# Kernel optimization log

Hardware: AMD Instinct MI355X
Metric: run time of the kernel (lower is better)

The kernel has to match this reference:

```python
import jax, jax.numpy as jnp
import numpy as np

B, N, D_IN, D_HID = 8, 2048, 512, 512

def setup_inputs() -> dict:
    key = jax.random.key(0)
    k1, k2, k3 = jax.random.split(key, 3)
    inp = jax.random.normal(k1, (B, N, D_IN), dtype=jnp.float32)
    # nn.Linear(input_size, hidden_size): weight [hidden, in], bias [hidden]
    W = jax.random.normal(k2, (D_HID, D_IN), dtype=jnp.float32) * (1.0 / np.sqrt(D_IN))
    b = jax.random.normal(k3, (D_HID,), dtype=jnp.float32) * 0.01
    return {"input": inp, "W": W, "b": b}

def reference(input, W, b):
    # x = fc(input): [B, N, D_HID]
    x = jnp.einsum('bnd,hd->bnh', input, W) + b
    # scores = x @ x^T (NO scale factor, matching the original): [B, N, N]
    scores = jnp.einsum('bnh,bmh->bnm', x, x)
    attn = jax.nn.softmax(scores, axis=2)
    # output = attn @ raw input (V = input, not the projection): [B, N, D_IN]
    output = jnp.einsum('bnm,bmd->bnd', attn, input)
    return output
```

## Files before the change

kernel.cpp:

```cpp
#include <hip/hip_runtime.h>
#include <hip/hip_bf16.h>
#include <stdint.h>

typedef short vbf16x8 __attribute__((ext_vector_type(8)));
typedef float vf32x4 __attribute__((ext_vector_type(4)));
typedef unsigned short u16;

__device__ __forceinline__ float bf2f(u16 u) {
  union { unsigned int i; float f; } v; v.i = ((unsigned int)u) << 16; return v.f;
}
__device__ __forceinline__ u16 f2bf(float f) {
  union { float f; unsigned int i; } v; v.f = f;
  return (u16)((v.i + 0x7fffu + ((v.i >> 16) & 1u)) >> 16);
}
__device__ __forceinline__ void gld16(const void* g, void* l) {
  __builtin_amdgcn_global_load_lds((const __attribute__((address_space(1))) void*)g,
                                   (__attribute__((address_space(3))) void*)l, 16, 0, 0);
}
template<int N> __device__ __forceinline__ void wait_vmcnt() {
  asm volatile("s_waitcnt vmcnt(%0)" :: "n"(N) : "memory");
}
__device__ __forceinline__ vbf16x8 ldsv(const u16* p) { return *(const vbf16x8*)p; }

__global__ __launch_bounds__(256) void k_convw(const float* __restrict__ W, u16* __restrict__ Wb) {
  int i = blockIdx.x * 256 + threadIdx.x;
  float4 x = ((const float4*)W)[i];
  ushort4 h;
  h.x = f2bf(x.x); h.y = f2bf(x.y); h.z = f2bf(x.z); h.w = f2bf(x.w);
  ((ushort4*)Wb)[i] = h;
}

__global__ __launch_bounds__(256) void k_prep(const float* __restrict__ in,
                                              u16* __restrict__ Abf, u16* __restrict__ Vt) {
  __shared__ u16 Ts[64][72];
  const int tid = threadIdx.x;
  const int n0 = blockIdx.x * 64, d0 = blockIdx.y * 64, b = blockIdx.z;
  const float* src = in + ((long long)b * 2048 + n0) * 512 + d0;
#pragma unroll
  for (int j = 0; j < 4; ++j) {
    int chunk = tid + 256 * j;
    int r = chunk >> 4, c = (chunk & 15) * 4;
    float4 x = *(const float4*)(src + (long long)r * 512 + c);
    ushort4 h;
    h.x = f2bf(x.x); h.y = f2bf(x.y); h.z = f2bf(x.z); h.w = f2bf(x.w);
    *(ushort4*)(Abf + ((long long)b * 2048 + n0 + r) * 512 + d0 + c) = h;
    Ts[c + 0][r] = h.x; Ts[c + 1][r] = h.y; Ts[c + 2][r] = h.z; Ts[c + 3][r] = h.w;
  }
  __syncthreads();
#pragma unroll
  for (int j = 0; j < 2; ++j) {
    int chunk = tid + 256 * j;
    int dr = chunk >> 3, c8 = (chunk & 7) * 8;
    vbf16x8 w = *(const vbf16x8*)&Ts[dr][c8];
    *(vbf16x8*)(Vt + ((long long)b * 512 + d0 + dr) * 2048 + n0 + c8) = w;
  }
}

template<int NF, int PART>
__device__ __forceinline__ void stage_part(int tile, int NT, const u16* gA, const u16* gB,
                                           u16* As, u16* Bs, int rA, int colsw, int K, int wv) {
  if (tile >= NT) return;
  constexpr int kh = PART >> 1;
  constexpr int isB = PART & 1;
  const int buf = tile & 1;
  const int k0 = tile * 64 + kh * 32;
  if constexpr (!isB) {
    const u16* src = gA + (long long)rA * K + k0 + colsw;
    u16* dst = As + (buf * 2 + kh) * 8192 + wv * 512;
    gld16(src, dst);
    gld16(src + 128LL * K, dst + 4096);
  } else {
    constexpr int BN = 64 * NF;
    const u16* src = gB + (long long)rA * K + k0 + colsw;
    u16* dst = Bs + (buf * 2 + kh) * (BN * 32) + wv * 512;
    gld16(src, dst);
    if constexpr (NF == 4) gld16(src + 128LL * K, dst + 4096);
  }
}

template<int NF, bool OUTBF, bool BIAS, int MAP>
__global__ __launch_bounds__(512, 2) void k_gemm8(const u16* __restrict__ A,
                                                  const u16* __restrict__ Bt,
                                                  const float* __restrict__ bias,
                                                  void* __restrict__ Cout,
                                                  int M, int N, int K,
                                                  long long sA, long long sB, long long sC) {
  static_assert(NF == 2 || NF == 4, "NF");
  constexpr int BN = 64 * NF;
  constexpr int LB = NF / 2;
  constexpr int V_MAIN = 4 + LB;
  constexpr int V_LAST = 2 + LB;
  __shared__ __align__(16) u16 As[2 * 2 * 256 * 32];
  __shared__ __align__(16) u16 Bs[2 * 2 * BN * 32];

  const int tid = threadIdx.x, lane = tid & 63, wv = tid >> 6;
  const int wr = wv >> 2, wc = wv & 3;

  const int lin = blockIdx.x;
  const int xcd = lin & 7, idx = lin >> 3;
  int zb, browi, bcoli;
  if constexpr (MAP == 0) { zb = xcd; browi = idx >> 3; bcoli = idx & 7; }
  else if constexpr (MAP == 1) { zb = 0; browi = xcd * 8 + (idx >> 2); bcoli = idx & 3; }
  else { zb = xcd; browi = idx >> 2; bcoli = idx & 3; }
  const int brow = browi * 256, bcol = bcoli * BN;
  const long long z = zb;

  const u16* gA = A + z * sA + (long long)brow * K;
  const u16* gB = Bt + z * sB + (long long)bcol * K;
  const int NT = K >> 6;

  const int rA = wv * 16 + (lane >> 2);
  const int colsw = (((lane & 3) ^ ((lane >> 3) & 3)) << 3);

  const int slotp = ((lane >> 4) ^ (((lane & 15) >> 1) & 3));
  const int rdoff = (lane & 15) * 32 + slotp * 8;

  vf32x4 acc[8][NF] = {};

  stage_part<NF, 0>(0, NT, gA, gB, As, Bs, rA, colsw, K, wv);
  stage_part<NF, 1>(0, NT, gA, gB, As, Bs, rA, colsw, K, wv);
  stage_part<NF, 2>(0, NT, gA, gB, As, Bs, rA, colsw, K, wv);
  stage_part<NF, 3>(0, NT, gA, gB, As, Bs, rA, colsw, K, wv);
  stage_part<NF, 0>(1, NT, gA, gB, As, Bs, rA, colsw, K, wv);

  for (int t = 0; t < NT; ++t) {
    const int buf = t & 1;
    const u16* Ak0 = As + (buf * 2 + 0) * 8192 + wr * 4096 + rdoff;
    const u16* Ak1 = As + (buf * 2 + 1) * 8192 + wr * 4096 + rdoff;
    const u16* Bk0 = Bs + (buf * 2 + 0) * (BN * 32) + wc * (16 * NF) * 32 + rdoff;
    const u16* Bk1 = Bs + (buf * 2 + 1) * (BN * 32) + wc * (16 * NF) * 32 + rdoff;
    vbf16x8 afr[4], bfr[NF];

    if (t < NT - 1) wait_vmcnt<V_MAIN>(); else wait_vmcnt<V_LAST>();
    __builtin_amdgcn_sched_barrier(0);
    __builtin_amdgcn_s_barrier();
    __builtin_amdgcn_sched_barrier(0);
#pragma unroll
    for (int n = 0; n < NF; ++n) bfr[n] = ldsv(Bk0 + n * 512);
#pragma unroll
    for (int i = 0; i < 4; ++i) afr[i] = ldsv(Ak0 + i * 512);
    stage_part<NF, 1>(t + 1, NT, gA, gB, As, Bs, rA, colsw, K, wv);
    __builtin_amdgcn_s_setprio(1);
#pragma unroll
    for (int i = 0; i < 4; ++i)
#pragma unroll
      for (int n = 0; n < NF; ++n)
        acc[i][n] = __builtin_amdgcn_mfma_f32_16x16x32_bf16(afr[i], bfr[n], acc[i][n], 0, 0, 0);
    __builtin_amdgcn_s_setprio(0);

#pragma unroll
    for (int i = 0; i < 4; ++i) afr[i] = ldsv(Ak0 + (4 + i) * 512);
    stage_part<NF, 2>(t + 1, NT, gA, gB, As, Bs, rA, colsw, K, wv);
    __builtin_amdgcn_s_setprio(1);
#pragma unroll
    for (int i = 0; i < 4; ++i)
#pragma unroll
      for (int n = 0; n < NF; ++n)
        acc[4 + i][n] = __builtin_amdgcn_mfma_f32_16x16x32_bf16(afr[i], bfr[n], acc[4 + i][n], 0, 0, 0);
    __builtin_amdgcn_s_setprio(0);

    if (t < NT - 1) wait_vmcnt<V_MAIN>(); else wait_vmcnt<0>();
    __builtin_amdgcn_sched_barrier(0);
    __builtin_amdgcn_s_barrier();
    __builtin_amdgcn_sched_barrier(0);
#pragma unroll
    for (int n = 0; n < NF; ++n) bfr[n] = ldsv(Bk1 + n * 512);
#pragma unroll
    for (int i = 0; i < 4; ++i) afr[i] = ldsv(Ak1 + i * 512);
    stage_part<NF, 3>(t + 1, NT, gA, gB, As, Bs, rA, colsw, K, wv);
    __builtin_amdgcn_s_setprio(1);
#pragma unroll
    for (int i = 0; i < 4; ++i)
#pragma unroll
      for (int n = 0; n < NF; ++n)
        acc[i][n] = __builtin_amdgcn_mfma_f32_16x16x32_bf16(afr[i], bfr[n], acc[i][n], 0, 0, 0);
    __builtin_amdgcn_s_setprio(0);

#pragma unroll
    for (int i = 0; i < 4; ++i) afr[i] = ldsv(Ak1 + (4 + i) * 512);
    stage_part<NF, 0>(t + 2, NT, gA, gB, As, Bs, rA, colsw, K, wv);
    __builtin_amdgcn_s_setprio(1);
#pragma unroll
    for (int i = 0; i < 4; ++i)
#pragma unroll
      for (int n = 0; n < NF; ++n)
        acc[4 + i][n] = __builtin_amdgcn_mfma_f32_16x16x32_bf16(afr[i], bfr[n], acc[4 + i][n], 0, 0, 0);
    __builtin_amdgcn_s_setprio(0);
  }

  const long long zc = z * sC;
#pragma unroll
  for (int m = 0; m < 8; ++m) {
    const int row0 = brow + wr * 128 + m * 16 + (lane >> 4) * 4;
#pragma unroll
    for (int n = 0; n < NF; ++n) {
      const int col = bcol + wc * (16 * NF) + n * 16 + (lane & 15);
      const float bv = BIAS ? bias[col] : 0.0f;
#pragma unroll
      for (int r = 0; r < 4; ++r) {
        const float v = acc[m][n][r] + bv;
        const long long off = zc + (long long)(row0 + r) * N + col;
        if (OUTBF) ((u16*)Cout)[off] = f2bf(v);
        else       ((float*)Cout)[off] = v;
      }
    }
  }
}

__global__ __launch_bounds__(256) void k_softmax(u16* __restrict__ P) {
  const long long row = blockIdx.x;
  u16* p = P + row * 2048;
  const int tid = threadIdx.x, lane = tid & 63, wv = tid >> 6;
  vbf16x8 v = ((const vbf16x8*)p)[tid];
  float f[8];
#pragma unroll
  for (int j = 0; j < 8; ++j) f[j] = bf2f((u16)v[j]);
  float m = f[0];
#pragma unroll
  for (int j = 1; j < 8; ++j) m = fmaxf(m, f[j]);
  for (int o = 1; o < 64; o <<= 1) m = fmaxf(m, __shfl_xor(m, o));
  __shared__ float redm[4], reds[4];
  if (lane == 0) redm[wv] = m;
  __syncthreads();
  m = fmaxf(fmaxf(redm[0], redm[1]), fmaxf(redm[2], redm[3]));
  float s = 0.0f;
#pragma unroll
  for (int j = 0; j < 8; ++j) { f[j] = __expf(f[j] - m); s += f[j]; }
  for (int o = 1; o < 64; o <<= 1) s += __shfl_xor(s, o);
  if (lane == 0) reds[wv] = s;
  __syncthreads();
  const float inv = 1.0f / (reds[0] + reds[1] + reds[2] + reds[3]);
#pragma unroll
  for (int j = 0; j < 8; ++j) v[j] = (short)f2bf(f[j] * inv);
  ((vbf16x8*)p)[tid] = v;
}

extern "C" void kernel_launch(void* const* d_in, const int* in_sizes, int n_in,
                              void* d_out, int out_size, void* d_ws, size_t ws_size,
                              hipStream_t stream) {
  const float* input = (const float*)d_in[0];
  const float* W     = (const float*)d_in[1];
  const float* bias  = (const float*)d_in[2];
  float* out = (float*)d_out;

  char* ws = (char*)d_ws;
  u16* Xbf = (u16*)(ws);
  u16* Vt  = (u16*)(ws + 16777216);
  u16* P   = (u16*)(ws + 2LL * 16777216);
  u16* Abf = (u16*)(ws + 2LL * 16777216);
  u16* Wb  = (u16*)(ws + 3LL * 16777216);

  k_convw<<<256, 256, 0, stream>>>(W, Wb);
  k_prep<<<dim3(32, 8, 8), 256, 0, stream>>>(input, Abf, Vt);
  k_gemm8<2, true, true, 1><<<256, 512, 0, stream>>>(
      Abf, Wb, bias, Xbf, 16384, 512, 512, 0, 0, 0);
  k_gemm8<4, true, false, 0><<<512, 512, 0, stream>>>(
      Xbf, Xbf, nullptr, P, 2048, 2048, 512,
      2048LL * 512, 2048LL * 512, 2048LL * 2048);
  k_softmax<<<16384, 256, 0, stream>>>(P);
  k_gemm8<2, false, false, 2><<<256, 512, 0, stream>>>(
      P, Vt, nullptr, out, 2048, 512, 2048,
      2048LL * 2048, 512LL * 2048, 2048LL * 512);
}
```

Baseline: 133.4 us.

## Restage GEMM tiles as full 64-wide K rows with XOR swizzle and new prefetch schedule

Changes the shared-memory layout of the bf16 GEMM from two 32-wide K halves to one 64-column tile per buffer, using an 8-way XOR swizzle for async global-to-LDS loads and matching fragment reads. The prefetch of the next tile is redistributed over the four MFMA phases. Explicit lgkmcnt waits and extra workgroup barriers are added around each phase. The aim is fewer bank conflicts and wider contiguous global loads per row, at the cost of more barriers per K step.

Result: slower. 157.0 us (+17.8%).

```diff
diff --git a/kernel.cpp b/kernel.cpp
--- a/kernel.cpp
+++ b/kernel.cpp
@@ -19,6 +19,9 @@
 }
 template<int N> __device__ __forceinline__ void wait_vmcnt() {
   asm volatile("s_waitcnt vmcnt(%0)" :: "n"(N) : "memory");
+}
+__device__ __forceinline__ void lgkm0() {
+  asm volatile("s_waitcnt lgkmcnt(0)" ::: "memory");
 }
 __device__ __forceinline__ vbf16x8 ldsv(const u16* p) { return *(const vbf16x8*)p; }
 
@@ -56,26 +59,9 @@
   }
 }
 
-template<int NF, int PART>
-__device__ __forceinline__ void stage_part(int tile, int NT, const u16* gA, const u16* gB,
-                                           u16* As, u16* Bs, int rA, int colsw, int K, int wv) {
-  if (tile >= NT) return;
-  constexpr int kh = PART >> 1;
-  constexpr int isB = PART & 1;
-  const int buf = tile & 1;
-  const int k0 = tile * 64 + kh * 32;
-  if constexpr (!isB) {
-    const u16* src = gA + (long long)rA * K + k0 + colsw;
-    u16* dst = As + (buf * 2 + kh) * 8192 + wv * 512;
-    gld16(src, dst);
-    gld16(src + 128LL * K, dst + 4096);
-  } else {
-    constexpr int BN = 64 * NF;
-    const u16* src = gB + (long long)rA * K + k0 + colsw;
-    u16* dst = Bs + (buf * 2 + kh) * (BN * 32) + wv * 512;
-    gld16(src, dst);
-    if constexpr (NF == 4) gld16(src + 128LL * K, dst + 4096);
-  }
+__device__ __forceinline__ void sround(const u16* g, int K, int k0, u16* ldsbuf,
+                                       int r, int srow, int scol, int wv) {
+  gld16(g + (long long)(r * 64 + srow) * K + k0 + scol, ldsbuf + r * 4096 + wv * 512);
 }
 
 template<int NF, bool OUTBF, bool BIAS, int MAP>
@@ -87,11 +73,8 @@
                                                   long long sA, long long sB, long long sC) {
   static_assert(NF == 2 || NF == 4, "NF");
   constexpr int BN = 64 * NF;
-  constexpr int LB = NF / 2;
-  constexpr int V_MAIN = 4 + LB;
-  constexpr int V_LAST = 2 + LB;
-  __shared__ __align__(16) u16 As[2 * 2 * 256 * 32];
-  __shared__ __align__(16) u16 Bs[2 * 2 * BN * 32];
+  __shared__ __align__(16) u16 As[2 * 256 * 64];
+  __shared__ __align__(16) u16 Bs[2 * BN * 64];
 
   const int tid = threadIdx.x, lane = tid & 63, wv = tid >> 6;
   const int wr = wv >> 2, wc = wv & 3;
@@ -109,37 +92,47 @@
   const u16* gB = Bt + z * sB + (long long)bcol * K;
   const int NT = K >> 6;
 
-  const int rA = wv * 16 + (lane >> 2);
-  const int colsw = (((lane & 3) ^ ((lane >> 3) & 3)) << 3);
-
-  const int slotp = ((lane >> 4) ^ (((lane & 15) >> 1) & 3));
-  const int rdoff = (lane & 15) * 32 + slotp * 8;
+  const int srow = wv * 8 + (lane >> 3);
+  const int scol = (((lane & 7) ^ ((lane >> 3) & 7)) << 3);
+
+  const int rd0 = (lane & 15) * 64 + ((((lane >> 4)) ^ (lane & 7)) << 3);
+  const int wrb = wr * 8192;
+  const int wcb = wc * NF * 1024;
 
   vf32x4 acc[8][NF] = {};
-
-  stage_part<NF, 0>(0, NT, gA, gB, As, Bs, rA, colsw, K, wv);
-  stage_part<NF, 1>(0, NT, gA, gB, As, Bs, rA, colsw, K, wv);
-  stage_part<NF, 2>(0, NT, gA, gB, As, Bs, rA, colsw, K, wv);
-  stage_part<NF, 3>(0, NT, gA, gB, As, Bs, rA, colsw, K, wv);
-  stage_part<NF, 0>(1, NT, gA, gB, As, Bs, rA, colsw, K, wv);
+  vbf16x8 afr[4], bfr[NF];
+
+  sround(gA, K, 0, As, 0, srow, scol, wv);
+  sround(gA, K, 0, As, 1, srow, scol, wv);
+  sround(gA, K, 0, As, 2, srow, scol, wv);
+  sround(gA, K, 0, As, 3, srow, scol, wv);
+  sround(gB, K, 0, Bs, 0, srow, scol, wv);
+  sround(gB, K, 0, Bs, 1, srow, scol, wv);
+  if constexpr (NF == 4) {
+    sround(gB, K, 0, Bs, 2, srow, scol, wv);
+    sround(gB, K, 0, Bs, 3, srow, scol, wv);
+  }
 
   for (int t = 0; t < NT; ++t) {
     const int buf = t & 1;
-    const u16* Ak0 = As + (buf * 2 + 0) * 8192 + wr * 4096 + rdoff;
-    const u16* Ak1 = As + (buf * 2 + 1) * 8192 + wr * 4096 + rdoff;
-    const u16* Bk0 = Bs + (buf * 2 + 0) * (BN * 32) + wc * (16 * NF) * 32 + rdoff;
-    const u16* Bk1 = Bs + (buf * 2 + 1) * (BN * 32) + wc * (16 * NF) * 32 + rdoff;
-    vbf16x8 afr[4], bfr[NF];
-
-    if (t < NT - 1) wait_vmcnt<V_MAIN>(); else wait_vmcnt<V_LAST>();
-    __builtin_amdgcn_sched_barrier(0);
-    __builtin_amdgcn_s_barrier();
-    __builtin_amdgcn_sched_barrier(0);
-#pragma unroll
-    for (int n = 0; n < NF; ++n) bfr[n] = ldsv(Bk0 + n * 512);
-#pragma unroll
-    for (int i = 0; i < 4; ++i) afr[i] = ldsv(Ak0 + i * 512);
-    stage_part<NF, 1>(t + 1, NT, gA, gB, As, Bs, rA, colsw, K, wv);
+    const u16* Ar = As + buf * 16384;
+    const u16* Br = Bs + buf * (BN * 64);
+    u16* Ad = As + (buf ^ 1) * 16384;
+    u16* Bd = Bs + (buf ^ 1) * (BN * 64);
+    const int k1 = (t + 1) * 64;
+    const bool st = (t + 1 < NT);
+
+    if (st) { sround(gA, K, k1, Ad, 0, srow, scol, wv); sround(gA, K, k1, Ad, 1, srow, scol, wv); }
+    if (t < NT - 1) wait_vmcnt<2>(); else wait_vmcnt<0>();
+    __builtin_amdgcn_sched_barrier(0);
+    __builtin_amdgcn_s_barrier();
+    __builtin_amdgcn_sched_barrier(0);
+#pragma unroll
+    for (int n = 0; n < NF; ++n) bfr[n] = ldsv(Br + wcb + n * 1024 + rd0);
+#pragma unroll
+    for (int i = 0; i < 4; ++i) afr[i] = ldsv(Ar + wrb + i * 1024 + rd0);
+    lgkm0();
+    __builtin_amdgcn_sched_barrier(0);
     __builtin_amdgcn_s_setprio(1);
 #pragma unroll
     for (int i = 0; i < 4; ++i)
@@ -147,10 +140,18 @@
       for (int n = 0; n < NF; ++n)
         acc[i][n] = __builtin_amdgcn_mfma_f32_16x16x32_bf16(afr[i], bfr[n], acc[i][n], 0, 0, 0);
     __builtin_amdgcn_s_setprio(0);
-
-#pragma unroll
-    for (int i = 0; i < 4; ++i) afr[i] = ldsv(Ak0 + (4 + i) * 512);
-    stage_part<NF, 2>(t + 1, NT, gA, gB, As, Bs, rA, colsw, K, wv);
+    __builtin_amdgcn_s_barrier();
+
+#pragma unroll
+    for (int i = 0; i < 4; ++i) afr[i] = ldsv(Ar + wrb + (4 + i) * 1024 + rd0);
+    if (st) {
+      sround(gA, K, k1, Ad, 2, srow, scol, wv);
+      if constexpr (NF == 4) sround(gA, K, k1, Ad, 3, srow, scol, wv);
+    }
+    __builtin_amdgcn_sched_barrier(0);
+    __builtin_amdgcn_s_barrier();
+    lgkm0();
+    __builtin_amdgcn_sched_barrier(0);
     __builtin_amdgcn_s_setprio(1);
 #pragma unroll
     for (int i = 0; i < 4; ++i)
@@ -158,16 +159,23 @@
       for (int n = 0; n < NF; ++n)
         acc[4 + i][n] = __builtin_amdgcn_mfma_f32_16x16x32_bf16(afr[i], bfr[n], acc[4 + i][n], 0, 0, 0);
     __builtin_amdgcn_s_setprio(0);
-
-    if (t < NT - 1) wait_vmcnt<V_MAIN>(); else wait_vmcnt<0>();
-    __builtin_amdgcn_sched_barrier(0);
-    __builtin_amdgcn_s_barrier();
-    __builtin_amdgcn_sched_barrier(0);
-#pragma unroll
-    for (int n = 0; n < NF; ++n) bfr[n] = ldsv(Bk1 + n * 512);
-#pragma unroll
-    for (int i = 0; i < 4; ++i) afr[i] = ldsv(Ak1 + i * 512);
-    stage_part<NF, 3>(t + 1, NT, gA, gB, As, Bs, rA, colsw, K, wv);
+    __builtin_amdgcn_s_barrier();
+
+#pragma unroll
+    for (int n = 0; n < NF; ++n) bfr[n] = ldsv(Br + wcb + n * 1024 + (rd0 ^ 32));
+#pragma unroll
+    for (int i = 0; i < 4; ++i) afr[i] = ldsv(Ar + wrb + i * 1024 + (rd0 ^ 32));
+    if (st) {
+      if constexpr (NF == 4) {
+        sround(gB, K, k1, Bd, 0, srow, scol, wv); sround(gB, K, k1, Bd, 1, srow, scol, wv);
+      } else {
+        sround(gA, K, k1, Ad, 3, srow, scol, wv); sround(gB, K, k1, Bd, 0, srow, scol, wv);
+      }
+    }
+    __builtin_amdgcn_sched_barrier(0);
+    __builtin_amdgcn_s_barrier();
+    lgkm0();
+    __builtin_amdgcn_sched_barrier(0);
     __builtin_amdgcn_s_setprio(1);
 #pragma unroll
     for (int i = 0; i < 4; ++i)
@@ -175,10 +183,21 @@
       for (int n = 0; n < NF; ++n)
         acc[i][n] = __builtin_amdgcn_mfma_f32_16x16x32_bf16(afr[i], bfr[n], acc[i][n], 0, 0, 0);
     __builtin_amdgcn_s_setprio(0);
-
-#pragma unroll
-    for (int i = 0; i < 4; ++i) afr[i] = ldsv(Ak1 + (4 + i) * 512);
-    stage_part<NF, 0>(t + 2, NT, gA, gB, As, Bs, rA, colsw, K, wv);
+    __builtin_amdgcn_s_barrier();
+
+#pragma unroll
+    for (int i = 0; i < 4; ++i) afr[i] = ldsv(Ar + wrb + (4 + i) * 1024 + (rd0 ^ 32));
+    if (st) {
+      if constexpr (NF == 4) {
+        sround(gB, K, k1, Bd, 2, srow, scol, wv); sround(gB, K, k1, Bd, 3, srow, scol, wv);
+      } else {
+        sround(gB, K, k1, Bd, 1, srow, scol, wv);
+      }
+    }
+    __builtin_amdgcn_sched_barrier(0);
+    __builtin_amdgcn_s_barrier();
+    lgkm0();
+    __builtin_amdgcn_sched_barrier(0);
     __builtin_amdgcn_s_setprio(1);
 #pragma unroll
     for (int i = 0; i < 4; ++i)
@@ -186,6 +205,7 @@
       for (int n = 0; n < NF; ++n)
         acc[4 + i][n] = __builtin_amdgcn_mfma_f32_16x16x32_bf16(afr[i], bfr[n], acc[4 + i][n], 0, 0, 0);
     __builtin_amdgcn_s_setprio(0);
+    __builtin_amdgcn_s_barrier();
   }
 
   const long long zc = z * sC;
```

## Rewrite GEMM with triple-buffered 64-wide K tiles and fixed 256x128 block

Applied to the files above, without the earlier changes.

Replaces the double-buffered, half-K-split staging with a three-stage LDS ring buffer holding full 64-wide K tiles, prefetching two tiles ahead and rotating buffer pointers each iteration. This lets one barrier per K tile replace two. The LDS swizzle and read offsets change to match the 64-column row layout. The scores GEMM drops from a 256-wide N tile to 128, doubling its grid to 1024 blocks. The design aims to hide more global-load latency and cut barrier count, at the cost of more LDS per block and more B reloads for the scores GEMM.

Measured after the change: 125.3 us. 1.06x faster.

```diff
diff --git a/kernel.cpp b/kernel.cpp
--- a/kernel.cpp
+++ b/kernel.cpp
@@ -56,42 +56,20 @@
   }
 }
 
-template<int NF, int PART>
-__device__ __forceinline__ void stage_part(int tile, int NT, const u16* gA, const u16* gB,
-                                           u16* As, u16* Bs, int rA, int colsw, int K, int wv) {
-  if (tile >= NT) return;
-  constexpr int kh = PART >> 1;
-  constexpr int isB = PART & 1;
-  const int buf = tile & 1;
-  const int k0 = tile * 64 + kh * 32;
-  if constexpr (!isB) {
-    const u16* src = gA + (long long)rA * K + k0 + colsw;
-    u16* dst = As + (buf * 2 + kh) * 8192 + wv * 512;
-    gld16(src, dst);
-    gld16(src + 128LL * K, dst + 4096);
-  } else {
-    constexpr int BN = 64 * NF;
-    const u16* src = gB + (long long)rA * K + k0 + colsw;
-    u16* dst = Bs + (buf * 2 + kh) * (BN * 32) + wv * 512;
-    gld16(src, dst);
-    if constexpr (NF == 4) gld16(src + 128LL * K, dst + 4096);
-  }
-}
-
-template<int NF, bool OUTBF, bool BIAS, int MAP>
-__global__ __launch_bounds__(512, 2) void k_gemm8(const u16* __restrict__ A,
-                                                  const u16* __restrict__ Bt,
-                                                  const float* __restrict__ bias,
-                                                  void* __restrict__ Cout,
-                                                  int M, int N, int K,
-                                                  long long sA, long long sB, long long sC) {
-  static_assert(NF == 2 || NF == 4, "NF");
-  constexpr int BN = 64 * NF;
-  constexpr int LB = NF / 2;
-  constexpr int V_MAIN = 4 + LB;
-  constexpr int V_LAST = 2 + LB;
-  __shared__ __align__(16) u16 As[2 * 2 * 256 * 32];
-  __shared__ __align__(16) u16 Bs[2 * 2 * BN * 32];
+__device__ __forceinline__ void sround(const u16* g, int K, int k0, u16* ldsbuf,
+                                       int r, int srow, int scol, int wv) {
+  gld16(g + (long long)(r * 64 + srow) * K + k0 + scol, ldsbuf + r * 4096 + wv * 512);
+}
+
+template<bool OUTBF, bool BIAS, int MAP>
+__global__ __launch_bounds__(512, 2) void k_gemm(const u16* __restrict__ A,
+                                                 const u16* __restrict__ Bt,
+                                                 const float* __restrict__ bias,
+                                                 void* __restrict__ Cout,
+                                                 int M, int N, int K,
+                                                 long long sA, long long sB, long long sC) {
+  __shared__ __align__(16) u16 As[3 * 16384];
+  __shared__ __align__(16) u16 Bs[3 * 8192];
 
   const int tid = threadIdx.x, lane = tid & 63, wv = tid >> 6;
   const int wr = wv >> 2, wc = wv & 3;
@@ -99,93 +77,101 @@
   const int lin = blockIdx.x;
   const int xcd = lin & 7, idx = lin >> 3;
   int zb, browi, bcoli;
-  if constexpr (MAP == 0) { zb = xcd; browi = idx >> 3; bcoli = idx & 7; }
+  if constexpr (MAP == 0) { zb = xcd; browi = idx >> 4; bcoli = idx & 15; }
   else if constexpr (MAP == 1) { zb = 0; browi = xcd * 8 + (idx >> 2); bcoli = idx & 3; }
   else { zb = xcd; browi = idx >> 2; bcoli = idx & 3; }
-  const int brow = browi * 256, bcol = bcoli * BN;
+  const int brow = browi * 256, bcol = bcoli * 128;
   const long long z = zb;
 
   const u16* gA = A + z * sA + (long long)brow * K;
   const u16* gB = Bt + z * sB + (long long)bcol * K;
   const int NT = K >> 6;
 
-  const int rA = wv * 16 + (lane >> 2);
-  const int colsw = (((lane & 3) ^ ((lane >> 3) & 3)) << 3);
-
-  const int slotp = ((lane >> 4) ^ (((lane & 15) >> 1) & 3));
-  const int rdoff = (lane & 15) * 32 + slotp * 8;
-
-  vf32x4 acc[8][NF] = {};
-
-  stage_part<NF, 0>(0, NT, gA, gB, As, Bs, rA, colsw, K, wv);
-  stage_part<NF, 1>(0, NT, gA, gB, As, Bs, rA, colsw, K, wv);
-  stage_part<NF, 2>(0, NT, gA, gB, As, Bs, rA, colsw, K, wv);
-  stage_part<NF, 3>(0, NT, gA, gB, As, Bs, rA, colsw, K, wv);
-  stage_part<NF, 0>(1, NT, gA, gB, As, Bs, rA, colsw, K, wv);
+  const int srow = wv * 8 + (lane >> 3);
+  const int scol = (((lane & 7) ^ ((lane >> 3) & 7)) << 3);
+
+  const int rd0 = (lane & 15) * 64 + ((((lane >> 4)) ^ (lane & 7)) << 3);
+  const int wrb = wr * 8192;
+  const int wcb = wc * 2048;
+
+  vf32x4 acc[8][2] = {};
+  vbf16x8 afr[4], bfr[2];
+
+  u16 *A0 = As, *A1 = As + 16384, *A2 = As + 32768;
+  u16 *B0 = Bs, *B1 = Bs + 8192, *B2 = Bs + 16384;
+
+  sround(gA, K, 0, A0, 0, srow, scol, wv);
+  sround(gA, K, 0, A0, 1, srow, scol, wv);
+  sround(gA, K, 0, A0, 2, srow, scol, wv);
+  sround(gA, K, 0, A0, 3, srow, scol, wv);
+  sround(gB, K, 0, B0, 0, srow, scol, wv);
+  sround(gB, K, 0, B0, 1, srow, scol, wv);
+  sround(gA, K, 64, A1, 0, srow, scol, wv);
+  sround(gA, K, 64, A1, 1, srow, scol, wv);
+  sround(gA, K, 64, A1, 2, srow, scol, wv);
+  sround(gA, K, 64, A1, 3, srow, scol, wv);
+  sround(gB, K, 64, B1, 0, srow, scol, wv);
+  sround(gB, K, 64, B1, 1, srow, scol, wv);
 
   for (int t = 0; t < NT; ++t) {
-    const int buf = t & 1;
-    const u16* Ak0 = As + (buf * 2 + 0) * 8192 + wr * 4096 + rdoff;
-    const u16* Ak1 = As + (buf * 2 + 1) * 8192 + wr * 4096 + rdoff;
-    const u16* Bk0 = Bs + (buf * 2 + 0) * (BN * 32) + wc * (16 * NF) * 32 + rdoff;
-    const u16* Bk1 = Bs + (buf * 2 + 1) * (BN * 32) + wc * (16 * NF) * 32 + rdoff;
-    vbf16x8 afr[4], bfr[NF];
-
-    if (t < NT - 1) wait_vmcnt<V_MAIN>(); else wait_vmcnt<V_LAST>();
+    const int k2 = (t + 2) * 64;
+    const bool st = (t + 2 < NT);
+
+    if (t < NT - 1) wait_vmcnt<6>(); else wait_vmcnt<0>();
     __builtin_amdgcn_sched_barrier(0);
     __builtin_amdgcn_s_barrier();
     __builtin_amdgcn_sched_barrier(0);
-#pragma unroll
-    for (int n = 0; n < NF; ++n) bfr[n] = ldsv(Bk0 + n * 512);
-#pragma unroll
-    for (int i = 0; i < 4; ++i) afr[i] = ldsv(Ak0 + i * 512);
-    stage_part<NF, 1>(t + 1, NT, gA, gB, As, Bs, rA, colsw, K, wv);
-    __builtin_amdgcn_s_setprio(1);
-#pragma unroll
-    for (int i = 0; i < 4; ++i)
-#pragma unroll
-      for (int n = 0; n < NF; ++n)
+
+#pragma unroll
+    for (int n = 0; n < 2; ++n) bfr[n] = ldsv(B0 + wcb + n * 1024 + rd0);
+#pragma unroll
+    for (int i = 0; i < 4; ++i) afr[i] = ldsv(A0 + wrb + i * 1024 + rd0);
+    if (st) { sround(gA, K, k2, A2, 0, srow, scol, wv); sround(gA, K, k2, A2, 1, srow, scol, wv); }
+    __builtin_amdgcn_s_setprio(1);
+#pragma unroll
+    for (int i = 0; i < 4; ++i)
+#pragma unroll
+      for (int n = 0; n < 2; ++n)
         acc[i][n] = __builtin_amdgcn_mfma_f32_16x16x32_bf16(afr[i], bfr[n], acc[i][n], 0, 0, 0);
     __builtin_amdgcn_s_setprio(0);
 
 #pragma unroll
-    for (int i = 0; i < 4; ++i) afr[i] = ldsv(Ak0 + (4 + i) * 512);
-    stage_part<NF, 2>(t + 1, NT, gA, gB, As, Bs, rA, colsw, K, wv);
-    __builtin_amdgcn_s_setprio(1);
-#pragma unroll
-    for (int i = 0; i < 4; ++i)
-#pragma unroll
-      for (int n = 0; n < NF; ++n)
+    for (int i = 0; i < 4; ++i) afr[i] = ldsv(A0 + wrb + (4 + i) * 1024 + rd0);
+    if (st) sround(gA, K, k2, A2, 2, srow, scol, wv);
+    __builtin_amdgcn_s_setprio(1);
+#pragma unroll
+    for (int i = 0; i < 4; ++i)
+#pragma unroll
+      for (int n = 0; n < 2; ++n)
         acc[4 + i][n] = __builtin_amdgcn_mfma_f32_16x16x32_bf16(afr[i], bfr[n], acc[4 + i][n], 0, 0, 0);
     __builtin_amdgcn_s_setprio(0);
 
-    if (t < NT - 1) wait_vmcnt<V_MAIN>(); else wait_vmcnt<0>();
-    __builtin_amdgcn_sched_barrier(0);
-    __builtin_amdgcn_s_barrier();
-    __builtin_amdgcn_sched_barrier(0);
-#pragma unroll
-    for (int n = 0; n < NF; ++n) bfr[n] = ldsv(Bk1 + n * 512);
-#pragma unroll
-    for (int i = 0; i < 4; ++i) afr[i] = ldsv(Ak1 + i * 512);
-    stage_part<NF, 3>(t + 1, NT, gA, gB, As, Bs, rA, colsw, K, wv);
-    __builtin_amdgcn_s_setprio(1);
-#pragma unroll
-    for (int i = 0; i < 4; ++i)
-#pragma unroll
-      for (int n = 0; n < NF; ++n)
+#pragma unroll
+    for (int n = 0; n < 2; ++n) bfr[n] = ldsv(B0 + wcb + n * 1024 + (rd0 ^ 32));
+#pragma unroll
+    for (int i = 0; i < 4; ++i) afr[i] = ldsv(A0 + wrb + i * 1024 + (rd0 ^ 32));
+    if (st) { sround(gA, K, k2, A2, 3, srow, scol, wv); sround(gB, K, k2, B2, 0, srow, scol, wv); }
+    __builtin_amdgcn_s_setprio(1);
+#pragma unroll
+    for (int i = 0; i < 4; ++i)
+#pragma unroll
+      for (int n = 0; n < 2; ++n)
         acc[i][n] = __builtin_amdgcn_mfma_f32_16x16x32_bf16(afr[i], bfr[n], acc[i][n], 0, 0, 0);
     __builtin_amdgcn_s_setprio(0);
 
 #pragma unroll
-    for (int i = 0; i < 4; ++i) afr[i] = ldsv(Ak1 + (4 + i) * 512);
-    stage_part<NF, 0>(t + 2, NT, gA, gB, As, Bs, rA, colsw, K, wv);
-    __builtin_amdgcn_s_setprio(1);
-#pragma unroll
-    for (int i = 0; i < 4; ++i)
-#pragma unroll
-      for (int n = 0; n < NF; ++n)
+    for (int i = 0; i < 4; ++i) afr[i] = ldsv(A0 + wrb + (4 + i) * 1024 + (rd0 ^ 32));
+    if (st) sround(gB, K, k2, B2, 1, srow, scol, wv);
+    __builtin_amdgcn_s_setprio(1);
+#pragma unroll
+    for (int i = 0; i < 4; ++i)
+#pragma unroll
+      for (int n = 0; n < 2; ++n)
         acc[4 + i][n] = __builtin_amdgcn_mfma_f32_16x16x32_bf16(afr[i], bfr[n], acc[4 + i][n], 0, 0, 0);
     __builtin_amdgcn_s_setprio(0);
+
+    u16* ta = A0; A0 = A1; A1 = A2; A2 = ta;
+    u16* tb = B0; B0 = B1; B1 = B2; B2 = tb;
   }
 
   const long long zc = z * sC;
@@ -193,8 +179,8 @@
   for (int m = 0; m < 8; ++m) {
     const int row0 = brow + wr * 128 + m * 16 + (lane >> 4) * 4;
 #pragma unroll
-    for (int n = 0; n < NF; ++n) {
-      const int col = bcol + wc * (16 * NF) + n * 16 + (lane & 15);
+    for (int n = 0; n < 2; ++n) {
+      const int col = bcol + wc * 32 + n * 16 + (lane & 15);
       const float bv = BIAS ? bias[col] : 0.0f;
 #pragma unroll
       for (int r = 0; r < 4; ++r) {
@@ -252,13 +238,13 @@
 
   k_convw<<<256, 256, 0, stream>>>(W, Wb);
   k_prep<<<dim3(32, 8, 8), 256, 0, stream>>>(input, Abf, Vt);
-  k_gemm8<2, true, true, 1><<<256, 512, 0, stream>>>(
+  k_gemm<true, true, 1><<<256, 512, 0, stream>>>(
       Abf, Wb, bias, Xbf, 16384, 512, 512, 0, 0, 0);
-  k_gemm8<4, true, false, 0><<<512, 512, 0, stream>>>(
+  k_gemm<true, false, 0><<<1024, 512, 0, stream>>>(
       Xbf, Xbf, nullptr, P, 2048, 2048, 512,
       2048LL * 512, 2048LL * 512, 2048LL * 2048);
   k_softmax<<<16384, 256, 0, stream>>>(P);
-  k_gemm8<2, false, false, 2><<<256, 512, 0, stream>>>(
+  k_gemm<false, false, 2><<<256, 512, 0, stream>>>(
       P, Vt, nullptr, out, 2048, 512, 2048,
       2048LL * 2048, 512LL * 2048, 2048LL * 512);
 }
```
